# Kernel optimization log

Hardware: AMD Instinct MI355X
Metric: run time of the kernel (lower is better)

## Reference

```python
import jax, jax.numpy as jnp
import numpy as np

B, C, H, W = 16, 256, 64, 64

def setup_inputs() -> dict:
    key = jax.random.key(0)
    ks = jax.random.split(key, 4)
    scale = 1.0 / np.sqrt(C)
    return {
        "x": jax.random.normal(ks[0], (B, C, H, W), dtype=jnp.float32),
        "w1": jax.random.normal(ks[1], (C, C), dtype=jnp.float32) * scale,
        "b1": jnp.zeros((C,), dtype=jnp.float32),
        "w2": jax.random.normal(ks[2], (C, C), dtype=jnp.float32) * scale,
        "b2": jnp.zeros((C,), dtype=jnp.float32),
        "w3": jax.random.normal(ks[3], (C, C), dtype=jnp.float32) * scale,
        "b3": jnp.zeros((C,), dtype=jnp.float32),
    }

def reference(x, w1, b1, w2, b2, w3, b3):
    b, c, h, w = x.shape
    n = h * w
    # 1x1 convs == per-pixel linear maps over channels; w has shape [C_out, C_in]
    def proj(wt, bias):
        return jnp.einsum('bchw,oc->bohw', x, wt) + bias[None, :, None, None]
    v = proj(w1, b1).reshape(b, c, n).transpose(0, 2, 1)   # [B, N, C]
    q = proj(w2, b2).reshape(b, c, n)                      # [B, C, N]
    k = proj(w3, b3).reshape(b, c, n)                      # [B, C, N]
    weight = jnp.einsum('bcn,bdn->bcd', q, k)              # [B, C, C]
    # global softmax over the entire flattened C*C matrix per batch element
    weight = jax.nn.softmax(weight.reshape(b, -1), axis=1).reshape(b, c, c)
    out = jnp.einsum('bnc,bcd->bdn', v, weight)            # [B, C, N]
    return out.reshape(x.shape)
```

## Files before the change

### kernel.cpp

```cpp
#include <hip/hip_runtime.h>


typedef unsigned short u16;
typedef __attribute__((ext_vector_type(8))) short short8;
typedef __attribute__((ext_vector_type(4))) float floatx4;

__device__ __forceinline__ u16 f2b(float f) {
  union { float f; unsigned int u; } v; v.f = f;
  unsigned int u = v.u;
  return (u16)((u + 0x7fffu + ((u >> 16) & 1u)) >> 16);
}
__device__ __forceinline__ float b2f(u16 h) {
  union { unsigned int u; float f; } v; v.u = ((unsigned int)h) << 16;
  return v.f;
}
__device__ __forceinline__ unsigned int cvt_pk_bf16(float lo, float hi) {
  unsigned int r;
  asm("v_cvt_pk_bf16_f32 %0, %1, %2" : "=v"(r) : "v"(lo), "v"(hi));
  return r;
}

__global__ __launch_bounds__(256) void prep_w_kernel(
    const float* __restrict__ w1, const float* __restrict__ w2, const float* __restrict__ w3,
    u16* __restrict__ W1Th, u16* __restrict__ W2h, u16* __restrict__ W2l,
    u16* __restrict__ W3h, u16* __restrict__ W3l, float* __restrict__ xsum) {
  const int blk = blockIdx.x, t = threadIdx.x;
  if (blk == 576) {
#pragma unroll
    for (int i = 0; i < 16; ++i) xsum[t + i * 256] = 0.f;
    return;
  }
  if (blk < 64) {
    __shared__ float tile[32][33];
    const int e0 = (blk & 7) * 32, c0 = (blk >> 3) * 32;
    const int tx = t & 31, ty = t >> 5;
#pragma unroll
    for (int i = 0; i < 4; ++i)
      tile[ty + i * 8][tx] = w1[(c0 + ty + i * 8) * 256 + e0 + tx];
    __syncthreads();
#pragma unroll
    for (int i = 0; i < 4; ++i)
      W1Th[(e0 + ty + i * 8) * 256 + c0 + tx] = f2b(tile[tx][ty + i * 8]);
  } else {
    const int i = (blk - 64) * 256 + t;
    const int e = i & 0xffff;
    const float f = (i >> 16) ? w3[e] : w2[e];
    u16 h = f2b(f);
    if (i >> 16) { W3h[e] = h; W3l[e] = f2b(f - b2f(h)); }
    else         { W2h[e] = h; W2l[e] = f2b(f - b2f(h)); }
  }
}

__device__ __forceinline__ void stage8(const float4 a, const float4 b,
                                       u16* dH, u16* dL, float& xa) {
  const float f[8] = {a.x, a.y, a.z, a.w, b.x, b.y, b.z, b.w};
  union { unsigned int w[4]; uint4 q; } uh, ul;
#pragma unroll
  for (int i = 0; i < 4; ++i) {
    const unsigned int h = cvt_pk_bf16(f[2 * i], f[2 * i + 1]);
    uh.w[i] = h;
    union { unsigned int u; float ff; } h0, h1;
    h0.u = h << 16;
    h1.u = h & 0xffff0000u;
    ul.w[i] = cvt_pk_bf16(f[2 * i] - h0.ff, f[2 * i + 1] - h1.ff);
    xa += f[2 * i] + f[2 * i + 1];
  }
  *(uint4*)dH = uh.q;
  *(uint4*)dL = ul.q;
}

__global__ __launch_bounds__(512, 4) void gram_kernel(
    const float* __restrict__ x, float* __restrict__ Gp, float* __restrict__ xsum) {
  __shared__ u16 lH[2][256 * 32], lL[2][256 * 32];
  const int b = blockIdx.x >> 5, s = (blockIdx.x >> 1) & 15, mh = blockIdx.x & 1;
  const float* Xb = x + (long)b * 1048576 + s * 256;
  const int t = threadIdx.x;
  const int lane = t & 63, wave = t >> 6;
  const int quad = lane >> 4, l16 = lane & 15;
  const int wml = (wave & 1) * 64 + mh * 128;
  const int wn = (wave >> 1) * 64;
  const int r0 = t >> 2, qc = (t & 3) * 8;
  const int r1 = r0 + 128;
  const int wq = (((t & 3) ^ ((r0 >> 1) & 3))) * 8;
  const int rq = ((quad ^ ((l16 >> 1) & 3))) * 8;
  floatx4 acc[4][4] = {};
  float xa0 = 0.f, xa1 = 0.f;
  float4 p[4];
  p[0] = *(const float4*)(Xb + (long)r0 * 4096 + qc);
  p[1] = *(const float4*)(Xb + (long)r0 * 4096 + qc + 4);
  p[2] = *(const float4*)(Xb + (long)r1 * 4096 + qc);
  p[3] = *(const float4*)(Xb + (long)r1 * 4096 + qc + 4);
  stage8(p[0], p[1], lH[0] + r0 * 32 + wq, lL[0] + r0 * 32 + wq, xa0);
  stage8(p[2], p[3], lH[0] + r1 * 32 + wq, lL[0] + r1 * 32 + wq, xa1);
  __syncthreads();
  for (int kb = 0; kb < 8; ++kb) {
    const int cur = kb & 1, nxt = cur ^ 1;
    if (kb < 7) {
      const long kk = (kb + 1) * 32;
      p[0] = *(const float4*)(Xb + (long)r0 * 4096 + kk + qc);
      p[1] = *(const float4*)(Xb + (long)r0 * 4096 + kk + qc + 4);
      p[2] = *(const float4*)(Xb + (long)r1 * 4096 + kk + qc);
      p[3] = *(const float4*)(Xb + (long)r1 * 4096 + kk + qc + 4);
    }
    const u16* cH = lH[cur];
    const u16* cL = lL[cur];
    short8 ah[4], al[4];
#pragma unroll
    for (int i = 0; i < 4; ++i) {
      ah[i] = *(const short8*)(cH + (wml + i * 16 + l16) * 32 + rq);
      al[i] = *(const short8*)(cL + (wml + i * 16 + l16) * 32 + rq);
    }
#pragma unroll
    for (int j = 0; j < 4; ++j) {
      const short8 bh = *(const short8*)(cH + (wn + j * 16 + l16) * 32 + rq);
      const short8 bl = *(const short8*)(cL + (wn + j * 16 + l16) * 32 + rq);
#pragma unroll
      for (int i = 0; i < 4; ++i) {
        acc[i][j] = __builtin_amdgcn_mfma_f32_16x16x32_bf16(ah[i], bh, acc[i][j], 0, 0, 0);
        acc[i][j] = __builtin_amdgcn_mfma_f32_16x16x32_bf16(ah[i], bl, acc[i][j], 0, 0, 0);
        acc[i][j] = __builtin_amdgcn_mfma_f32_16x16x32_bf16(al[i], bh, acc[i][j], 0, 0, 0);
      }
    }
    if (kb < 7) {
      stage8(p[0], p[1], lH[nxt] + r0 * 32 + wq, lL[nxt] + r0 * 32 + wq, xa0);
      stage8(p[2], p[3], lH[nxt] + r1 * 32 + wq, lL[nxt] + r1 * 32 + wq, xa1);
    }
    __syncthreads();
  }
  if (mh == 0) {
    float v = xa0;
    v += __shfl_xor(v, 1);
    v += __shfl_xor(v, 2);
    if ((t & 3) == 0) atomicAdd(&xsum[b * 256 + r0], v);
    v = xa1;
    v += __shfl_xor(v, 1);
    v += __shfl_xor(v, 2);
    if ((t & 3) == 0) atomicAdd(&xsum[b * 256 + r1], v);
  }
  float* G = Gp + ((long)b * 16 + s) * 65536;
#pragma unroll
  for (int i = 0; i < 4; ++i) {
    const int row0 = wml + i * 16 + quad * 4;
#pragma unroll
    for (int j = 0; j < 4; ++j) {
      const int col = wn + j * 16 + l16;
#pragma unroll
      for (int r = 0; r < 4; ++r)
        G[(long)(row0 + r) * 256 + col] = acc[i][j][r];
    }
  }
}

__global__ __launch_bounds__(256) void reduce_g_kernel(
    const float* __restrict__ Gp, u16* __restrict__ Gh, u16* __restrict__ Gl) {
  const long e = ((long)blockIdx.x * 256 + threadIdx.x) * 4;
  const long base = ((e >> 16) << 20) + (e & 65535);
  float4 s = {0.f, 0.f, 0.f, 0.f};
#pragma unroll
  for (int i = 0; i < 16; ++i) {
    const float4 v = *(const float4*)(Gp + base + (long)i * 65536);
    s.x += v.x; s.y += v.y; s.z += v.z; s.w += v.w;
  }
  union { u16 h[4]; uint2 q; } oh, ol;
  const float sv[4] = {s.x, s.y, s.z, s.w};
#pragma unroll
  for (int c = 0; c < 4; ++c) {
    const u16 h = f2b(sv[c]);
    oh.h[c] = h;
    ol.h[c] = f2b(sv[c] - b2f(h));
  }
  *(uint2*)(Gh + e) = oh.q;
  *(uint2*)(Gl + e) = ol.q;
}

template <bool X3, int EPI>
__global__ __launch_bounds__(256) void gemm_small(
    const u16* __restrict__ Ah, const u16* __restrict__ Al,
    const u16* __restrict__ Bh, const u16* __restrict__ Bl,
    long aBatch, long bBatch, long oBatch,
    float* __restrict__ outF, u16* __restrict__ outH, u16* __restrict__ outL) {
  constexpr int LR = 40;
  __shared__ u16 smem[(X3 ? 4 : 2) * 64 * LR];
  u16* lAh = smem;
  u16* lBh = smem + 64 * LR;
  u16* lAl = X3 ? (smem + 2 * 64 * LR) : nullptr;
  u16* lBl = X3 ? (smem + 3 * 64 * LR) : nullptr;
  const int b = blockIdx.z;
  const int tm = blockIdx.x & 3, tn = blockIdx.x >> 2;
  const u16* Ahb = Ah + (long)b * aBatch + (long)tm * 64 * 256;
  const u16* Bhb = Bh + (long)b * bBatch + (long)tn * 64 * 256;
  const u16* Alb = X3 ? (Al + (long)b * aBatch + (long)tm * 64 * 256) : nullptr;
  const u16* Blb = X3 ? (Bl + (long)b * bBatch + (long)tn * 64 * 256) : nullptr;
  const int t = threadIdx.x;
  const int lane = t & 63, wave = t >> 6;
  const int quad = lane >> 4, l16 = lane & 15;
  const int wm = (wave & 1) * 32, wn = (wave >> 1) * 32;
  const int r = t >> 2, qc = (t & 3) * 8;
  floatx4 acc[2][2] = {};
  uint4 pA, pB, pAl = {}, pBl = {};
  pA = *(const uint4*)(Ahb + (long)r * 256 + qc);
  pB = *(const uint4*)(Bhb + (long)r * 256 + qc);
  if (X3) {
    pAl = *(const uint4*)(Alb + (long)r * 256 + qc);
    pBl = *(const uint4*)(Blb + (long)r * 256 + qc);
  }
  for (int kk = 0; kk < 256; kk += 32) {
    __syncthreads();
    *(uint4*)(lAh + r * LR + qc) = pA;
    *(uint4*)(lBh + r * LR + qc) = pB;
    if (X3) {
      *(uint4*)(lAl + r * LR + qc) = pAl;
      *(uint4*)(lBl + r * LR + qc) = pBl;
    }
    __syncthreads();
    if (kk < 224) {
      pA = *(const uint4*)(Ahb + (long)r * 256 + kk + 32 + qc);
      pB = *(const uint4*)(Bhb + (long)r * 256 + kk + 32 + qc);
      if (X3) {
        pAl = *(const uint4*)(Alb + (long)r * 256 + kk + 32 + qc);
        pBl = *(const uint4*)(Blb + (long)r * 256 + kk + 32 + qc);
      }
    }
    short8 afh[2], bfh[2], afl[2], bfl[2];
#pragma unroll
    for (int i = 0; i < 2; ++i) {
      afh[i] = *(const short8*)(lAh + (wm + i * 16 + l16) * LR + quad * 8);
      bfh[i] = *(const short8*)(lBh + (wn + i * 16 + l16) * LR + quad * 8);
      if (X3) {
        afl[i] = *(const short8*)(lAl + (wm + i * 16 + l16) * LR + quad * 8);
        bfl[i] = *(const short8*)(lBl + (wn + i * 16 + l16) * LR + quad * 8);
      }
    }
#pragma unroll
    for (int i = 0; i < 2; ++i)
#pragma unroll
      for (int j = 0; j < 2; ++j) {
        acc[i][j] = __builtin_amdgcn_mfma_f32_16x16x32_bf16(afh[i], bfh[j], acc[i][j], 0, 0, 0);
        if (X3) {
          acc[i][j] = __builtin_amdgcn_mfma_f32_16x16x32_bf16(afh[i], bfl[j], acc[i][j], 0, 0, 0);
          acc[i][j] = __builtin_amdgcn_mfma_f32_16x16x32_bf16(afl[i], bfh[j], acc[i][j], 0, 0, 0);
        }
      }
  }
  const long obase = (long)b * oBatch;
#pragma unroll
  for (int i = 0; i < 2; ++i) {
    const int mb = tm * 64 + wm + i * 16 + quad * 4;
#pragma unroll
    for (int j = 0; j < 2; ++j) {
      const int n = tn * 64 + wn + j * 16 + l16;
#pragma unroll
      for (int rr = 0; rr < 4; ++rr) {
        const float v = acc[i][j][rr];
        const long idx = obase + (long)(mb + rr) * 256 + n;
        if (EPI == 0) {
          outF[idx] = v;
        } else if (EPI == 1) {
          u16 h = f2b(v);
          outH[idx] = h;
          outL[idx] = f2b(v - b2f(h));
        } else {
          outH[idx] = f2b(v);
        }
      }
    }
  }
}

__global__ __launch_bounds__(512, 2) void gemm_out(
    const u16* __restrict__ Mh, const float* __restrict__ x,
    const float* __restrict__ bb, float* __restrict__ out) {
  constexpr int LR = 40;
  __shared__ u16 lA[256 * LR], lB[128 * LR];
  const int b = blockIdx.z;
  const int tn = blockIdx.x;
  const u16* Ab = Mh + (long)b * 65536;
  const float* Xb = x + (long)b * 1048576 + tn * 128;
  const int t = threadIdx.x;
  const int lane = t & 63, wave = t >> 6;
  const int quad = lane >> 4, l16 = lane & 15;
  const int wm = (wave & 3) * 64;
  const int wn = (wave >> 2) * 64;
  const int erp = (t >> 5) * 2;
  const int n0 = (t & 31) * 4;
  const int ra = t >> 2, qc = (t & 3) * 8;
  floatx4 acc[4][4] = {};
  uint4 pA[2];
  float4 pb0, pb1;
#pragma unroll
  for (int h = 0; h < 2; ++h)
    pA[h] = *(const uint4*)(Ab + (long)(ra + h * 128) * 256 + qc);
  pb0 = *(const float4*)(Xb + (long)erp * 4096 + n0);
  pb1 = *(const float4*)(Xb + (long)(erp + 1) * 4096 + n0);
  for (int kk = 0; kk < 256; kk += 32) {
    __syncthreads();
#pragma unroll
    for (int h = 0; h < 2; ++h)
      *(uint4*)(lA + (ra + h * 128) * LR + qc) = pA[h];
    {
      const float fa[4] = {pb0.x, pb0.y, pb0.z, pb0.w};
      const float fc[4] = {pb1.x, pb1.y, pb1.z, pb1.w};
#pragma unroll
      for (int i = 0; i < 4; ++i) {
        const int nl = n0 + i;
        const int sb = (erp >> 3) ^ ((nl >> 4) & 3);
        *(unsigned int*)(lB + nl * LR + sb * 8 + (erp & 7)) =
            cvt_pk_bf16(fa[i], fc[i]);
      }
    }
    __syncthreads();
    if (kk < 224) {
      const int k2 = kk + 32;
#pragma unroll
      for (int h = 0; h < 2; ++h)
        pA[h] = *(const uint4*)(Ab + (long)(ra + h * 128) * 256 + k2 + qc);
      pb0 = *(const float4*)(Xb + (long)(k2 + erp) * 4096 + n0);
      pb1 = *(const float4*)(Xb + (long)(k2 + erp + 1) * 4096 + n0);
    }
    short8 af[4];
#pragma unroll
    for (int i = 0; i < 4; ++i)
      af[i] = *(const short8*)(lA + (wm + i * 16 + l16) * LR + quad * 8);
#pragma unroll
    for (int j = 0; j < 4; ++j) {
      const int n = wn + j * 16 + l16;
      const int rb = quad ^ ((n >> 4) & 3);
      const short8 bf = *(const short8*)(lB + n * LR + rb * 8);
#pragma unroll
      for (int i = 0; i < 4; ++i)
        acc[i][j] = __builtin_amdgcn_mfma_f32_16x16x32_bf16(af[i], bf, acc[i][j], 0, 0, 0);
    }
  }
  const long obase = (long)b * 1048576;
#pragma unroll
  for (int i = 0; i < 4; ++i) {
    const int mb = wm + i * 16 + quad * 4;
#pragma unroll
    for (int j = 0; j < 4; ++j) {
      const int n = tn * 128 + wn + j * 16 + l16;
#pragma unroll
      for (int r = 0; r < 4; ++r)
        out[obase + (long)(mb + r) * 4096 + n] = acc[i][j][r] + bb[b * 256 + mb + r];
    }
  }
}

__global__ __launch_bounds__(512) void bias_prep_kernel(
    const float* __restrict__ w2, const float* __restrict__ w3,
    const float* __restrict__ xsum, float* __restrict__ S2, float* __restrict__ S3) {
  __shared__ float xs[256];
  const int b = blockIdx.x, t = threadIdx.x;
  if (t < 256) xs[t] = xsum[b * 256 + t];
  __syncthreads();
  const float* wm = (t < 256) ? w2 : w3;
  const int a = t & 255;
  float s = 0.f;
#pragma unroll 4
  for (int c = 0; c < 256; ++c) s += wm[a * 256 + c] * xs[c];
  if (t < 256) S2[b * 256 + a] = s;
  else         S3[b * 256 + a] = s;
}

__global__ __launch_bounds__(256) void softmax_pass1(
    const float* __restrict__ Lt, const float* __restrict__ S2, const float* __restrict__ S3,
    const float* __restrict__ b2, const float* __restrict__ b3,
    float* __restrict__ bm, float* __restrict__ bs) {
  __shared__ float ls2[256], lb2[256];
  __shared__ float redm[4], reds[4];
  const int b = blockIdx.y, blk = blockIdx.x, t = threadIdx.x;
  ls2[t] = S2[b * 256 + t];
  lb2[t] = b2[t];
  __syncthreads();
  const int fw0 = blk * 2048 + t * 8;
  const int d = fw0 >> 8, a0 = fw0 & 255;
  const float c1 = b3[d];
  const float c0 = S3[b * 256 + d] + 4096.f * c1;
  const long base = (long)b * 65536 + fw0;
  float4 v0 = *(const float4*)(Lt + base);
  float4 v1 = *(const float4*)(Lt + base + 4);
  float v[8] = {v0.x, v0.y, v0.z, v0.w, v1.x, v1.y, v1.z, v1.w};
  float m = -3.4e38f;
#pragma unroll
  for (int i = 0; i < 8; ++i) {
    v[i] += lb2[a0 + i] * c0 + c1 * ls2[a0 + i];
    m = fmaxf(m, v[i]);
  }
  for (int o = 32; o; o >>= 1) m = fmaxf(m, __shfl_xor(m, o));
  const int wid = t >> 6, lane = t & 63;
  if (lane == 0) redm[wid] = m;
  __syncthreads();
  const float bmax = fmaxf(fmaxf(redm[0], redm[1]), fmaxf(redm[2], redm[3]));
  float s = 0.f;
#pragma unroll
  for (int i = 0; i < 8; ++i) s += __expf(v[i] - bmax);
  for (int o = 32; o; o >>= 1) s += __shfl_xor(s, o);
  if (lane == 0) reds[wid] = s;
  __syncthreads();
  if (t == 0) {
    bm[b * 32 + blk] = bmax;
    bs[b * 32 + blk] = reds[0] + reds[1] + reds[2] + reds[3];
  }
}

__global__ __launch_bounds__(256) void softmax_pass3(
    const float* __restrict__ Lt, const float* __restrict__ S2, const float* __restrict__ S3,
    const float* __restrict__ b2, const float* __restrict__ b3,
    const float* __restrict__ bm, const float* __restrict__ bs,
    const float* __restrict__ b1, u16* __restrict__ WTh, float* __restrict__ bb) {
  __shared__ float ls2[256], lb2[256], lb1[256];
  __shared__ float sM, sInv;
  const int b = blockIdx.y, blk = blockIdx.x, t = threadIdx.x;
  if (t < 64) {
    const float m = (t < 32) ? bm[b * 32 + t] : -3.4e38f;
    float s = (t < 32) ? bs[b * 32 + t] : 0.f;
    float M = m;
    for (int o = 32; o; o >>= 1) M = fmaxf(M, __shfl_xor(M, o));
    s *= __expf(m - M);
    for (int o = 32; o; o >>= 1) s += __shfl_xor(s, o);
    if (t == 0) { sM = M; sInv = 1.0f / s; }
  }
  ls2[t] = S2[b * 256 + t];
  lb2[t] = b2[t];
  lb1[t] = b1[t];
  __syncthreads();
  const float M = sM, inv = sInv;
  const int fw0 = blk * 2048 + t * 8;
  const int d = fw0 >> 8, a0 = fw0 & 255;
  const float c1 = b3[d];
  const float c0 = S3[b * 256 + d] + 4096.f * c1;
  const long base = (long)b * 65536 + fw0;
  float4 v0 = *(const float4*)(Lt + base);
  float4 v1 = *(const float4*)(Lt + base + 4);
  float v[8] = {v0.x, v0.y, v0.z, v0.w, v1.x, v1.y, v1.z, v1.w};
  union { u16 h[8]; uint4 q; } o;
  float bsum = 0.f;
#pragma unroll
  for (int i = 0; i < 8; ++i) {
    const float vv = v[i] + lb2[a0 + i] * c0 + c1 * ls2[a0 + i];
    const float w = __expf(vv - M) * inv;
    o.h[i] = f2b(w);
    bsum += w * lb1[a0 + i];
  }
  *(uint4*)(WTh + base) = o.q;
  for (int off = 16; off; off >>= 1) bsum += __shfl_xor(bsum, off);
  if ((t & 31) == 0) bb[b * 256 + d] = bsum;
}

extern "C" void kernel_launch(void* const* d_in, const int* in_sizes, int n_in,
                              void* d_out, int out_size, void* d_ws, size_t ws_size,
                              hipStream_t stream) {
  const float* x  = (const float*)d_in[0];
  const float* w1 = (const float*)d_in[1];
  const float* b1 = (const float*)d_in[2];
  const float* w2 = (const float*)d_in[3];
  const float* b2 = (const float*)d_in[4];
  const float* w3 = (const float*)d_in[5];
  const float* b3 = (const float*)d_in[6];
  float* out = (float*)d_out;

  char* ws = (char*)d_ws;
  size_t off = 0;
  auto alloc = [&](size_t bytes) {
    void* p = ws + off;
    off += (bytes + 255) & ~(size_t)255;
    return p;
  };
  float* Gp = (float*)alloc(16ull * 16 * 65536 * 4);
  float* xsum = (float*)alloc(16 * 256 * 4);
  u16* Gh   = (u16*)alloc(16ull * 65536 * 2);
  u16* Gl   = (u16*)alloc(16ull * 65536 * 2);
  u16* T3h  = (u16*)alloc(16ull * 65536 * 2);
  u16* T3l  = (u16*)alloc(16ull * 65536 * 2);
  float* Lb = (float*)alloc(16ull * 65536 * 4);
  u16* WTh  = (u16*)alloc(16ull * 65536 * 2);
  u16* Mh   = (u16*)alloc(16ull * 65536 * 2);
  u16* W1Th = (u16*)alloc(65536 * 2);
  u16* W2h  = (u16*)alloc(65536 * 2);
  u16* W2l  = (u16*)alloc(65536 * 2);
  u16* W3h  = (u16*)alloc(65536 * 2);
  u16* W3l  = (u16*)alloc(65536 * 2);
  float* S2   = (float*)alloc(16 * 256 * 4);
  float* S3   = (float*)alloc(16 * 256 * 4);
  float* bmx  = (float*)alloc(16 * 32 * 4);
  float* bsx  = (float*)alloc(16 * 32 * 4);
  float* bb   = (float*)alloc(16 * 256 * 4);

  prep_w_kernel<<<577, 256, 0, stream>>>(w1, w2, w3, W1Th, W2h, W2l, W3h, W3l, xsum);

  gram_kernel<<<512, 512, 0, stream>>>(x, Gp, xsum);
  reduce_g_kernel<<<1024, 256, 0, stream>>>(Gp, Gh, Gl);

  gemm_small<true, 1><<<dim3(16, 1, 16), 256, 0, stream>>>(
      W3h, W3l, Gh, Gl, 0, 65536, 65536, nullptr, T3h, T3l);
  gemm_small<true, 0><<<dim3(16, 1, 16), 256, 0, stream>>>(
      T3h, T3l, W2h, W2l, 65536, 0, 65536, Lb, nullptr, nullptr);

  bias_prep_kernel<<<16, 512, 0, stream>>>(w2, w3, xsum, S2, S3);
  softmax_pass1<<<dim3(32, 16), 256, 0, stream>>>(Lb, S2, S3, b2, b3, bmx, bsx);
  softmax_pass3<<<dim3(32, 16), 256, 0, stream>>>(Lb, S2, S3, b2, b3, bmx, bsx,
                                                  b1, WTh, bb);

  gemm_small<false, 2><<<dim3(16, 1, 16), 256, 0, stream>>>(
      WTh, nullptr, W1Th, nullptr, 65536, 0, 65536, nullptr, Mh, nullptr);
  gemm_out<<<dim3(32, 1, 16), 512, 0, stream>>>(Mh, x, bb, out);
}
```

Baseline: 231.1 us.

## Stream A tiles into double-buffered LDS with direct global-to-LDS loads in gemm_out

Loads of the bf16 attention-weight tile in gemm_out now use global_load_lds to write straight into a double-buffered, XOR-swizzled LDS buffer. This skips the register staging and the separate ds_write for A. The x tile loads change from float4 vectors to scalar strided loads. The aim is to cut VGPR pressure and LDS store instructions and to overlap A fetches with MFMA work. The cost is more scalar global loads for B, and correctness depends on the direct-LDS write layout and lane ordering.

```diff
diff --git a/kernel.cpp b/kernel.cpp
--- a/kernel.cpp
+++ b/kernel.cpp
@@ -18,6 +18,11 @@
   unsigned int r;
   asm("v_cvt_pk_bf16_f32 %0, %1, %2" : "=v"(r) : "v"(lo), "v"(hi));
   return r;
+}
+__device__ __forceinline__ void gload_lds16(const u16* g, u16* l) {
+  __builtin_amdgcn_global_load_lds(
+      (const __attribute__((address_space(1))) unsigned int*)(const void*)g,
+      (__attribute__((address_space(3))) unsigned int*)(void*)l, 16, 0, 0);
 }
 
 __global__ __launch_bounds__(256) void prep_w_kernel(
@@ -270,8 +275,8 @@
 __global__ __launch_bounds__(512, 2) void gemm_out(
     const u16* __restrict__ Mh, const float* __restrict__ x,
     const float* __restrict__ bb, float* __restrict__ out) {
-  constexpr int LR = 40;
-  __shared__ u16 lA[256 * LR], lB[128 * LR];
+  __shared__ u16 lA[2][256 * 32];
+  __shared__ u16 lB[128 * 40];
   const int b = blockIdx.z;
   const int tn = blockIdx.x;
   const u16* Ab = Mh + (long)b * 65536;
@@ -282,50 +287,53 @@
   const int wm = (wave & 3) * 64;
   const int wn = (wave >> 2) * 64;
   const int erp = (t >> 5) * 2;
-  const int n0 = (t & 31) * 4;
-  const int ra = t >> 2, qc = (t & 3) * 8;
+  const int n0 = t & 31;
+  const int ra = t >> 2;
+  const int sc = ((t & 3) ^ ((t >> 3) & 3)) * 8;
+  const int rqA = (quad ^ ((l16 >> 1) & 3)) * 8;
+  u16* wA0 = &lA[0][0] + wave * 16 * 32;
+  u16* wA1 = &lA[1][0] + wave * 16 * 32;
   floatx4 acc[4][4] = {};
-  uint4 pA[2];
-  float4 pb0, pb1;
-#pragma unroll
-  for (int h = 0; h < 2; ++h)
-    pA[h] = *(const uint4*)(Ab + (long)(ra + h * 128) * 256 + qc);
-  pb0 = *(const float4*)(Xb + (long)erp * 4096 + n0);
-  pb1 = *(const float4*)(Xb + (long)(erp + 1) * 4096 + n0);
-  for (int kk = 0; kk < 256; kk += 32) {
+  float pb[8];
+  gload_lds16(Ab + (long)ra * 256 + sc, wA0);
+  gload_lds16(Ab + (long)(ra + 128) * 256 + sc, wA0 + 128 * 32);
+#pragma unroll
+  for (int i = 0; i < 4; ++i) {
+    pb[i]     = Xb[(long)erp * 4096 + n0 + 32 * i];
+    pb[4 + i] = Xb[(long)(erp + 1) * 4096 + n0 + 32 * i];
+  }
+  for (int s = 0; s < 8; ++s) {
+    const int kk = s * 32;
+    const u16* curA = lA[s & 1];
     __syncthreads();
 #pragma unroll
-    for (int h = 0; h < 2; ++h)
-      *(uint4*)(lA + (ra + h * 128) * LR + qc) = pA[h];
-    {
-      const float fa[4] = {pb0.x, pb0.y, pb0.z, pb0.w};
-      const float fc[4] = {pb1.x, pb1.y, pb1.z, pb1.w};
+    for (int i = 0; i < 4; ++i) {
+      const int nl = n0 + 32 * i;
+      const int sb = (erp >> 3) ^ ((nl >> 4) & 3);
+      *(unsigned int*)(lB + nl * 40 + sb * 8 + (erp & 7)) =
+          cvt_pk_bf16(pb[i], pb[4 + i]);
+    }
+    __syncthreads();
+    if (s < 7) {
+      const int k2 = kk + 32;
+      u16* nA = (s & 1) ? wA0 : wA1;
+      gload_lds16(Ab + (long)ra * 256 + k2 + sc, nA);
+      gload_lds16(Ab + (long)(ra + 128) * 256 + k2 + sc, nA + 128 * 32);
 #pragma unroll
       for (int i = 0; i < 4; ++i) {
-        const int nl = n0 + i;
-        const int sb = (erp >> 3) ^ ((nl >> 4) & 3);
-        *(unsigned int*)(lB + nl * LR + sb * 8 + (erp & 7)) =
-            cvt_pk_bf16(fa[i], fc[i]);
+        pb[i]     = Xb[(long)(k2 + erp) * 4096 + n0 + 32 * i];
+        pb[4 + i] = Xb[(long)(k2 + erp + 1) * 4096 + n0 + 32 * i];
       }
     }
-    __syncthreads();
-    if (kk < 224) {
-      const int k2 = kk + 32;
-#pragma unroll
-      for (int h = 0; h < 2; ++h)
-        pA[h] = *(const uint4*)(Ab + (long)(ra + h * 128) * 256 + k2 + qc);
-      pb0 = *(const float4*)(Xb + (long)(k2 + erp) * 4096 + n0);
-      pb1 = *(const float4*)(Xb + (long)(k2 + erp + 1) * 4096 + n0);
-    }
     short8 af[4];
 #pragma unroll
     for (int i = 0; i < 4; ++i)
-      af[i] = *(const short8*)(lA + (wm + i * 16 + l16) * LR + quad * 8);
+      af[i] = *(const short8*)(curA + (wm + i * 16 + l16) * 32 + rqA);
 #pragma unroll
     for (int j = 0; j < 4; ++j) {
       const int n = wn + j * 16 + l16;
       const int rb = quad ^ ((n >> 4) & 3);
-      const short8 bf = *(const short8*)(lB + n * LR + rb * 8);
+      const short8 bf = *(const short8*)(lB + n * 40 + rb * 8);
 #pragma unroll
       for (int i = 0; i < 4; ++i)
         acc[i][j] = __builtin_amdgcn_mfma_f32_16x16x32_bf16(af[i], bf, acc[i][j], 0, 0, 0);
```

New measurement: 218.4 us. 1.06x faster.
